# Kernel optimization log

Measured on AMD Instinct MI355X. Metric: run time of the kernel, lower is better.

## Reference

```python
import jax, jax.numpy as jnp
import numpy as np

N_NODES = 100000
N_EDGES = 1600000
IN_CH = 128
HID = 64
N_CLASSES = 16
N_GRAPHS = 64


def setup_inputs() -> dict:
    key = jax.random.key(0)
    ks = jax.random.split(key, 10)
    x = jax.random.normal(ks[0], (N_NODES, IN_CH), dtype=jnp.float32)
    edge_index = jax.random.randint(ks[1], (2, N_EDGES), 0, N_NODES, dtype=jnp.int64)
    edge_weight = jax.random.uniform(ks[2], (N_EDGES,), dtype=jnp.float32)
    batch = jnp.sort(jax.random.randint(ks[3], (N_NODES,), 0, N_GRAPHS, dtype=jnp.int64))
    s1 = 1.0 / np.sqrt(IN_CH)
    s2 = 1.0 / np.sqrt(HID)
    W1 = jax.random.uniform(ks[4], (IN_CH, HID), jnp.float32, -s1, s1)
    b1 = jnp.zeros((HID,), jnp.float32)
    W2 = jax.random.uniform(ks[5], (HID, HID), jnp.float32, -s2, s2)
    b2 = jnp.zeros((HID,), jnp.float32)
    Wl = jax.random.uniform(ks[6], (HID, N_CLASSES), jnp.float32, -s2, s2)
    bl = jax.random.uniform(ks[7], (N_CLASSES,), jnp.float32, -s2, s2)
    return {"x": x, "edge_index": edge_index, "edge_weight": edge_weight,
            "batch": batch, "W1": W1, "b1": b1, "W2": W2, "b2": b2,
            "Wl": Wl, "bl": bl}


def _gcn_conv(x, src, dst, ew, W, b, n_nodes):
    # PyG GCNConv: h = x @ W; symmetric normalization with self-loops;
    # out[dst] += norm * h[src]; out += bias.
    deg = jax.ops.segment_sum(ew, dst, num_segments=n_nodes)
    deg_inv_sqrt = jnp.where(deg > 0, jax.lax.rsqrt(jnp.maximum(deg, 1e-30)), 0.0)
    norm = deg_inv_sqrt[src] * ew * deg_inv_sqrt[dst]  # [E']
    h = x @ W                                          # [N, out]
    msg = h[src] * norm[:, None]                       # [E', out] gather
    out = jax.ops.segment_sum(msg, dst, num_segments=n_nodes)  # scatter-add
    return out + b


def reference(x, edge_index, edge_weight, batch, W1, b1, W2, b2, Wl, bl):
    n = x.shape[0]
    # add self loops once (weight 1.0), shared by both conv layers
    loop = jnp.arange(n, dtype=edge_index.dtype)
    src = jnp.concatenate([edge_index[0], loop])
    dst = jnp.concatenate([edge_index[1], loop])
    ew = jnp.concatenate([edge_weight, jnp.ones((n,), edge_weight.dtype)])

    h = jax.nn.relu(_gcn_conv(x, src, dst, ew, W1, b1, n))
    h = jax.nn.relu(_gcn_conv(h, src, dst, ew, W2, b2, n))

    # global_mean_pool over graphs
    sums = jax.ops.segment_sum(h, batch, num_segments=N_GRAPHS)  # [G, HID]
    cnt = jax.ops.segment_sum(jnp.ones((n,), h.dtype), batch, num_segments=N_GRAPHS)
    pooled = sums / jnp.maximum(cnt, 1.0)[:, None]

    return pooled @ Wl + bl
```

## Files before the change

### kernel.cpp

```cpp
#include <hip/hip_runtime.h>
#include <hip/hip_fp16.h>

#define N_NODES   100000
#define N_EDGES   1600000
#define IN_CH     128
#define HID       64
#define N_CLASSES 16
#define N_GRAPHS  64

#define BK_SH     9
#define BK_NODES  512
#define NB        ((N_NODES + BK_NODES - 1) / BK_NODES)
#define BK_CAP    10240
#define CH_EDGES  4096
#define EPT       16
#define NCH       ((N_EDGES + CH_EDGES - 1) / CH_EDGES)
#define AGG_NPW   2

typedef __attribute__((ext_vector_type(8))) short bf16x8;
typedef __attribute__((ext_vector_type(4))) float f32x4;
typedef __attribute__((ext_vector_type(4))) unsigned u32x4;
typedef __attribute__((ext_vector_type(2))) unsigned u32x2;

__device__ __forceinline__ unsigned short f2bf(float f) {
    unsigned u = __float_as_uint(f);
    u += 0x7fffu + ((u >> 16) & 1u);
    return (unsigned short)(u >> 16);
}
__device__ __forceinline__ f32x4 bf4v(uint2 v) {
    u32x4 u;
    u.x = v.x << 16; u.y = v.x & 0xffff0000u;
    u.z = v.y << 16; u.w = v.y & 0xffff0000u;
    return __builtin_bit_cast(f32x4, u);
}
__device__ __forceinline__ float dec_ew(unsigned v) {
    return __half2float(__ushort_as_half((unsigned short)(v >> 17)));
}

#if __has_builtin(__builtin_amdgcn_make_buffer_rsrc) && \
    __has_builtin(__builtin_amdgcn_raw_buffer_load_b32) && \
    __has_builtin(__builtin_amdgcn_raw_buffer_load_b64)
struct BufView {
    __amdgpu_buffer_rsrc_t rsrc;
    __device__ __forceinline__ void init(const void* p) {
        rsrc = __builtin_amdgcn_make_buffer_rsrc((void*)p, (short)0,
                                                 (int)0xFFFFFFFF, 0x00020000);
    }
    __device__ __forceinline__ unsigned ld32(unsigned off) const {
        return __builtin_amdgcn_raw_buffer_load_b32(rsrc, (int)off, 0, 0);
    }
    __device__ __forceinline__ uint2 ld64(unsigned off) const {
        u32x2 r = __builtin_amdgcn_raw_buffer_load_b64(rsrc, (int)off, 0, 0);
        return make_uint2(r.x, r.y);
    }
};
#else
struct BufView {
    const char* base;
    __device__ __forceinline__ void init(const void* p) { base = (const char*)p; }
    __device__ __forceinline__ unsigned ld32(unsigned off) const {
        return *(const unsigned*)(base + off);
    }
    __device__ __forceinline__ uint2 ld64(unsigned off) const {
        return *(const uint2*)(base + off);
    }
};
#endif

__global__ void k_init(int* __restrict__ bcursor, float* __restrict__ pooled) {
    int i = blockIdx.x * 256 + threadIdx.x;
    if (i < NB) bcursor[i] = i * BK_CAP;
    if (i < N_GRAPHS * HID) pooled[i] = 0.0f;
}

__global__ void k_binscatter(const int* __restrict__ src, const int* __restrict__ dst,
                             const float* __restrict__ ew, int* __restrict__ bcursor,
                             int2* __restrict__ bedges) {
    __shared__ int  hist[NB];
    __shared__ int  offs[NB];
    __shared__ int  gbase[NB];
    __shared__ int  sc[256];
    __shared__ int2 stage[CH_EDGES];
    __shared__ int  dest[CH_EDGES];
    const int t = threadIdx.x;
    const int base = blockIdx.x * CH_EDGES;
    const int nloc = min(CH_EDGES, N_EDGES - base);

    for (int i = t; i < NB; i += 256) hist[i] = 0;
    __syncthreads();

    int myb[EPT], myr[EPT], myp[EPT]; float myw[EPT];
#pragma unroll
    for (int j = 0; j < EPT; ++j) {
        int i = base + j * 256 + t;
        if (i < N_EDGES) {
            int s = src[i], d = dst[i];
            int b = d >> BK_SH;
            myb[j] = b;
            myr[j] = atomicAdd(&hist[b], 1);
            myp[j] = s | ((d & (BK_NODES - 1)) << 17);
            myw[j] = ew[i];
        } else {
            myb[j] = -1;
        }
    }
    __syncthreads();

    int v = (t < NB) ? hist[t] : 0;
    sc[t] = v;
    __syncthreads();
    for (int off = 1; off < 256; off <<= 1) {
        int a = (t >= off) ? sc[t - off] : 0;
        __syncthreads();
        sc[t] += a;
        __syncthreads();
    }
    if (t < NB) {
        offs[t] = sc[t] - v;
        gbase[t] = (v > 0) ? atomicAdd(&bcursor[t], v) : 0;
    }
    __syncthreads();

#pragma unroll
    for (int j = 0; j < EPT; ++j) {
        if (myb[j] >= 0) {
            int p = offs[myb[j]] + myr[j];
            stage[p] = make_int2(myp[j], __float_as_int(myw[j]));
            dest[p] = gbase[myb[j]] + myr[j];
        }
    }
    __syncthreads();

    for (int i = t; i < nloc; i += 256)
        bedges[dest[i]] = stage[i];
}

__global__ __launch_bounds__(256) void k_build(const int* __restrict__ bcursor,
                                               const int2* __restrict__ bedges,
                                               int2* __restrict__ rowse,
                                               float* __restrict__ dis,
                                               unsigned* __restrict__ csr) {
    __shared__ int2  eds[BK_CAP];
    __shared__ int   cnt[BK_NODES];
    __shared__ float dsum[BK_NODES];
    __shared__ int   cur[BK_NODES];
    __shared__ int   sc[256];
    const int b = blockIdx.x;
    const int t = threadIdx.x;
    const int beg = b * BK_CAP, end = bcursor[b];
    const int n = end - beg;

    for (int i = t; i < BK_NODES; i += 256) { cnt[i] = 0; dsum[i] = 0.0f; }
    __syncthreads();

    for (int i = t; i < n; i += 256) {
        int2 e = bedges[beg + i];
        eds[i] = e;
        int dl = ((unsigned)e.x) >> 17;
        atomicAdd(&cnt[dl], 1);
        atomicAdd(&dsum[dl], __int_as_float(e.y));
    }
    __syncthreads();

    int a0 = cnt[2 * t], a1 = cnt[2 * t + 1];
    int pair = a0 + a1;
    sc[t] = pair;
    __syncthreads();
    for (int off = 1; off < 256; off <<= 1) {
        int a = (t >= off) ? sc[t - off] : 0;
        __syncthreads();
        sc[t] += a;
        __syncthreads();
    }
    int excl = sc[t] - pair;
    cur[2 * t] = excl;
    cur[2 * t + 1] = excl + a0;
    {
        int n0 = b * BK_NODES + 2 * t;
        if (n0 < N_NODES) {
            rowse[n0] = make_int2(beg + excl, beg + excl + a0);
            dis[n0] = rsqrtf(1.0f + dsum[2 * t]);
        }
        int n1 = n0 + 1;
        if (n1 < N_NODES) {
            rowse[n1] = make_int2(beg + excl + a0, beg + excl + a0 + a1);
            dis[n1] = rsqrtf(1.0f + dsum[2 * t + 1]);
        }
    }
    __syncthreads();

    for (int i = t; i < n; i += 256) {
        int2 e = eds[i];
        int dl = ((unsigned)e.x) >> 17;
        int s = e.x & 0x1FFFF;
        unsigned short w16 = __half_as_ushort(__float2half(__int_as_float(e.y)));
        int pos = beg + atomicAdd(&cur[dl], 1);
        csr[pos] = (unsigned)s | ((unsigned)w16 << 17);
    }
}

template <int K, bool INB>
__global__ __launch_bounds__(256) void k_gemm(const float* __restrict__ x,
                                              const unsigned short* __restrict__ xb,
                                              const float* __restrict__ W,
                                              const float* __restrict__ dis,
                                              unsigned short* __restrict__ hb) {
    constexpr int AS = K + 8;
    __shared__ unsigned short wt[64 * AS];
    const int t    = threadIdx.x;
    const int lane = t & 63;
    const int wave = t >> 6;
    const int m    = lane & 15;
    const int quad = lane >> 4;
    const int rowbase = blockIdx.x * 64;

    bf16x8 afrag[K / 32];

    if constexpr (!INB) {
        __shared__ unsigned short a_s[64 * AS];
        constexpr int CPR = K / 8;
        for (int c = t; c < 64 * CPR; c += 256) {
            int row = c / CPR, cc = c % CPR;
            int gr = rowbase + row;
            float4 v0, v1;
            if (gr < N_NODES) {
                v0 = *(const float4*)&x[(long)gr * K + cc * 8];
                v1 = *(const float4*)&x[(long)gr * K + cc * 8 + 4];
            } else {
                v0 = make_float4(0.f, 0.f, 0.f, 0.f); v1 = v0;
            }
            uint4 p;
            p.x = f2bf(v0.x) | ((unsigned)f2bf(v0.y) << 16);
            p.y = f2bf(v0.z) | ((unsigned)f2bf(v0.w) << 16);
            p.z = f2bf(v1.x) | ((unsigned)f2bf(v1.y) << 16);
            p.w = f2bf(v1.z) | ((unsigned)f2bf(v1.w) << 16);
            *(uint4*)&a_s[row * AS + cc * 8] = p;
        }
        for (int idx = t; idx < K * 64; idx += 256) {
            int k = idx >> 6, n = idx & 63;
            wt[n * AS + k] = f2bf(W[idx]);
        }
        __syncthreads();
#pragma unroll
        for (int ks = 0; ks < K / 32; ++ks)
            afrag[ks] = *(const bf16x8*)&a_s[(wave * 16 + m) * AS + ks * 32 + quad * 8];
    } else {
        const int gr = rowbase + wave * 16 + m;
#pragma unroll
        for (int ks = 0; ks < K / 32; ++ks) {
            if (gr < N_NODES)
                afrag[ks] = *(const bf16x8*)&xb[(long)gr * K + ks * 32 + quad * 8];
            else
                afrag[ks] = (bf16x8){0, 0, 0, 0, 0, 0, 0, 0};
        }
        for (int idx = t; idx < K * 64; idx += 256) {
            int k = idx >> 6, n = idx & 63;
            wt[n * AS + k] = f2bf(W[idx]);
        }
        __syncthreads();
    }

    bf16x8 bfrag[4][K / 32];
#pragma unroll
    for (int nt = 0; nt < 4; ++nt)
#pragma unroll
        for (int ks = 0; ks < K / 32; ++ks)
            bfrag[nt][ks] = *(const bf16x8*)&wt[(nt * 16 + m) * AS + ks * 32 + quad * 8];

    f32x4 acc[4];
#pragma unroll
    for (int nt = 0; nt < 4; ++nt) acc[nt] = (f32x4){0.f, 0.f, 0.f, 0.f};

#pragma unroll
    for (int ks = 0; ks < K / 32; ++ks) {
#pragma unroll
        for (int nt = 0; nt < 4; ++nt)
            acc[nt] = __builtin_amdgcn_mfma_f32_16x16x32_bf16(afrag[ks], bfrag[nt][ks],
                                                              acc[nt], 0, 0, 0);
    }

#pragma unroll
    for (int i = 0; i < 4; ++i) {
        int gr = rowbase + wave * 16 + quad * 4 + i;
        if (gr < N_NODES) {
            float dsc = dis[gr];
#pragma unroll
            for (int nt = 0; nt < 4; ++nt)
                hb[(long)gr * HID + nt * 16 + m] = f2bf(dsc * acc[nt][i]);
        }
    }
}


#define FULLBLK(pX, eX, f_, x0, x1, x2, x3, accX)                             \
    do {                                                                      \
        const unsigned e0_ = x0, e1_ = x1, e2_ = x2, e3_ = x3;                \
        pX += 16;                                                             \
        f_ = (pX + 16 <= eX);                                                 \
        if (f_) {                                                             \
            const unsigned v_ = (unsigned)((pX + g) << 2);                    \
            x0 = vc.ld32(v_);      x1 = vc.ld32(v_ + 16);                     \
            x2 = vc.ld32(v_ + 32); x3 = vc.ld32(v_ + 48);                     \
        }                                                                     \
        f32x4 v0_ = bf4v(vh.ld64(((e0_ & 0x1FFFF) << 7) | coff));             \
        f32x4 v1_ = bf4v(vh.ld64(((e1_ & 0x1FFFF) << 7) | coff));             \
        f32x4 v2_ = bf4v(vh.ld64(((e2_ & 0x1FFFF) << 7) | coff));             \
        f32x4 v3_ = bf4v(vh.ld64(((e3_ & 0x1FFFF) << 7) | coff));             \
        accX += v0_ * dec_ew(e0_);                                            \
        accX += v1_ * dec_ew(e1_);                                            \
        accX += v2_ * dec_ew(e2_);                                            \
        accX += v3_ * dec_ew(e3_);                                            \
    } while (0)

template <bool OB>
__global__ void k_aggregate(const int2* __restrict__ rowse,
                            const unsigned* __restrict__ csr,
                            const uint2* __restrict__ hb, const float* __restrict__ dis,
                            const float* __restrict__ b, const int* __restrict__ batch,
                            float* __restrict__ pooled, uint2* __restrict__ outb) {
    __shared__ float psh[4 * AGG_NPW][HID];
    const int tid  = threadIdx.x;
    const int lane = tid & 63;
    const int g    = lane >> 4;
    const int c4   = lane & 15;
    const int wave = tid >> 6;
    const int node0 = (blockIdx.x * 4 + wave) * AGG_NPW;
    const int node1 = node0 + 1;
    const float4 bb = ((const float4*)b)[c4];
    const f32x4 bbv = {bb.x, bb.y, bb.z, bb.w};

    BufView vc; vc.init(csr);
    BufView vh; vh.init(hb);
    const unsigned coff = (unsigned)(c4 << 3);

    const int4 rr = *(const int4*)&rowse[node0];
    const uint2 hs0 = hb[node0 * 16 + c4];
    const uint2 hs1 = hb[node1 * 16 + c4];

    f32x4 acc0 = (g == 0) ? bf4v(hs0) : (f32x4){0.f, 0.f, 0.f, 0.f};
    f32x4 acc1 = (g == 0) ? bf4v(hs1) : (f32x4){0.f, 0.f, 0.f, 0.f};

    int p0 = rr.x; const int e0 = rr.y;
    int p1 = rr.z; const int e1 = rr.w;

    unsigned a0 = 0, a1 = 0, a2 = 0, a3 = 0;
    unsigned b0 = 0, b1 = 0, b2 = 0, b3 = 0;
    bool fA = (p0 + 16 <= e0);
    bool fB = (p1 + 16 <= e1);
    if (fA) {
        const unsigned v = (unsigned)((p0 + g) << 2);
        a0 = vc.ld32(v);      a1 = vc.ld32(v + 16);
        a2 = vc.ld32(v + 32); a3 = vc.ld32(v + 48);
    }
    if (fB) {
        const unsigned v = (unsigned)((p1 + g) << 2);
        b0 = vc.ld32(v);      b1 = vc.ld32(v + 16);
        b2 = vc.ld32(v + 32); b3 = vc.ld32(v + 48);
    }

    while (fA && fB) {
        FULLBLK(p0, e0, fA, a0, a1, a2, a3, acc0);
        FULLBLK(p1, e1, fB, b0, b1, b2, b3, acc1);
    }
    while (fA) FULLBLK(p0, e0, fA, a0, a1, a2, a3, acc0);
    while (fB) FULLBLK(p1, e1, fB, b0, b1, b2, b3, acc1);

    const bool tA = (p0 < e0);
    const bool tB = (p1 < e1);
    unsigned ta0 = 0, ta1 = 0, ta2 = 0, ta3 = 0;
    unsigned tb0 = 0, tb1 = 0, tb2 = 0, tb3 = 0;
    if (tA) {
        const int last = e0 - 1;
        ta0 = vc.ld32((unsigned)(min(p0 + g,      last) << 2));
        ta1 = vc.ld32((unsigned)(min(p0 + 4 + g,  last) << 2));
        ta2 = vc.ld32((unsigned)(min(p0 + 8 + g,  last) << 2));
        ta3 = vc.ld32((unsigned)(min(p0 + 12 + g, last) << 2));
    }
    if (tB) {
        const int last = e1 - 1;
        tb0 = vc.ld32((unsigned)(min(p1 + g,      last) << 2));
        tb1 = vc.ld32((unsigned)(min(p1 + 4 + g,  last) << 2));
        tb2 = vc.ld32((unsigned)(min(p1 + 8 + g,  last) << 2));
        tb3 = vc.ld32((unsigned)(min(p1 + 12 + g, last) << 2));
    }
    if (tA) {
        f32x4 v0 = bf4v(vh.ld64(((ta0 & 0x1FFFF) << 7) | coff));
        f32x4 v1 = bf4v(vh.ld64(((ta1 & 0x1FFFF) << 7) | coff));
        f32x4 v2 = bf4v(vh.ld64(((ta2 & 0x1FFFF) << 7) | coff));
        f32x4 v3 = bf4v(vh.ld64(((ta3 & 0x1FFFF) << 7) | coff));
        acc0 += v0 * ((p0 + g      < e0) ? dec_ew(ta0) : 0.f);
        acc0 += v1 * ((p0 + 4 + g  < e0) ? dec_ew(ta1) : 0.f);
        acc0 += v2 * ((p0 + 8 + g  < e0) ? dec_ew(ta2) : 0.f);
        acc0 += v3 * ((p0 + 12 + g < e0) ? dec_ew(ta3) : 0.f);
    }
    if (tB) {
        f32x4 v0 = bf4v(vh.ld64(((tb0 & 0x1FFFF) << 7) | coff));
        f32x4 v1 = bf4v(vh.ld64(((tb1 & 0x1FFFF) << 7) | coff));
        f32x4 v2 = bf4v(vh.ld64(((tb2 & 0x1FFFF) << 7) | coff));
        f32x4 v3 = bf4v(vh.ld64(((tb3 & 0x1FFFF) << 7) | coff));
        acc1 += v0 * ((p1 + g      < e1) ? dec_ew(tb0) : 0.f);
        acc1 += v1 * ((p1 + 4 + g  < e1) ? dec_ew(tb1) : 0.f);
        acc1 += v2 * ((p1 + 8 + g  < e1) ? dec_ew(tb2) : 0.f);
        acc1 += v3 * ((p1 + 12 + g < e1) ? dec_ew(tb3) : 0.f);
    }

#pragma unroll
    for (int i = 0; i < 4; ++i) {
        float t0 = acc0[i];
        t0 += __shfl_xor(t0, 16); t0 += __shfl_xor(t0, 32);
        acc0[i] = t0;
        float t1 = acc1[i];
        t1 += __shfl_xor(t1, 16); t1 += __shfl_xor(t1, 32);
        acc1[i] = t1;
    }

    if (g == 0) {
        const float dd0 = dis[node0];
        const float dd1 = dis[node1];
        f32x4 o0 = acc0 * dd0 + bbv;
        f32x4 o1 = acc1 * dd1 + bbv;
        o0.x = fmaxf(o0.x, 0.f); o0.y = fmaxf(o0.y, 0.f);
        o0.z = fmaxf(o0.z, 0.f); o0.w = fmaxf(o0.w, 0.f);
        o1.x = fmaxf(o1.x, 0.f); o1.y = fmaxf(o1.y, 0.f);
        o1.z = fmaxf(o1.z, 0.f); o1.w = fmaxf(o1.w, 0.f);
        if constexpr (OB) {
            uint2 pk0, pk1;
            pk0.x = (unsigned)f2bf(o0.x) | ((unsigned)f2bf(o0.y) << 16);
            pk0.y = (unsigned)f2bf(o0.z) | ((unsigned)f2bf(o0.w) << 16);
            pk1.x = (unsigned)f2bf(o1.x) | ((unsigned)f2bf(o1.y) << 16);
            pk1.y = (unsigned)f2bf(o1.z) | ((unsigned)f2bf(o1.w) << 16);
            outb[node0 * 16 + c4] = pk0;
            outb[node1 * 16 + c4] = pk1;
        } else {
            *(f32x4*)&psh[wave * AGG_NPW][c4 * 4] = o0;
            *(f32x4*)&psh[wave * AGG_NPW + 1][c4 * 4] = o1;
        }
    }

    if constexpr (!OB) {
        __syncthreads();
        if (tid < HID) {
            const int nb0 = blockIdx.x * 4 * AGG_NPW;
            int curg = batch[nb0];
            float a = 0.f;
#pragma unroll
            for (int j = 0; j < 4 * AGG_NPW; ++j) {
                int bg = batch[nb0 + j];
                if (bg != curg) {
                    atomicAdd(&pooled[curg * HID + tid], a);
                    a = 0.f; curg = bg;
                }
                a += psh[j][tid];
            }
            atomicAdd(&pooled[curg * HID + tid], a);
        }
    }
}

__global__ __launch_bounds__(1024) void k_out(const float* __restrict__ pooled,
                      const int* __restrict__ batch,
                      const float* __restrict__ Wl, const float* __restrict__ bl,
                      float* __restrict__ out) {
    __shared__ int bnd[N_GRAPHS + 1];
    int tid = threadIdx.x;
    if (tid <= N_GRAPHS) {
        int target = tid;
        int lo = 0, hi = N_NODES;
        while (lo < hi) {
            int mid = (lo + hi) >> 1;
            if (batch[mid] < target) lo = mid + 1; else hi = mid;
        }
        bnd[tid] = lo;
    }
    __syncthreads();
    int g = tid >> 4, k = tid & 15;
    float cntg = (float)(bnd[g + 1] - bnd[g]);
    float inv = 1.0f / fmaxf(cntg, 1.0f);
    float acc = 0.f;
#pragma unroll
    for (int h = 0; h < HID; ++h) acc += pooled[g * HID + h] * Wl[h * N_CLASSES + k];
    out[g * N_CLASSES + k] = acc * inv + bl[k];
}

extern "C" void kernel_launch(void* const* d_in, const int* in_sizes, int n_in,
                              void* d_out, int out_size, void* d_ws, size_t ws_size,
                              hipStream_t stream) {
    const float* x     = (const float*)d_in[0];
    const int*   ei    = (const int*)d_in[1];
    const float* ew    = (const float*)d_in[2];
    const int*   batch = (const int*)d_in[3];
    const float* W1    = (const float*)d_in[4];
    const float* b1    = (const float*)d_in[5];
    const float* W2    = (const float*)d_in[6];
    const float* b2    = (const float*)d_in[7];
    const float* Wl    = (const float*)d_in[8];
    const float* bl    = (const float*)d_in[9];

    const int* srcv = ei;
    const int* dstv = ei + N_EDGES;

    char* wsb = (char*)d_ws;
    float*          dis    = (float*)wsb;              wsb += 100352 * 4;
    int2*           rowse  = (int2*)wsb;               wsb += 100352 * 8;
    int*            bcursor= (int*)wsb;                wsb += 256 * 4;
    unsigned*       csr    = (unsigned*)wsb;           wsb += (size_t)NB * BK_CAP * 4;
    unsigned short* hb     = (unsigned short*)wsb;     wsb += N_NODES * HID * 2;
    char*           scratch= wsb;                      wsb += N_NODES * HID * 4;
    float*          pooled = (float*)wsb;              wsb += N_GRAPHS * HID * 4;
    float*          out    = (float*)d_out;
    int2*           bedges = (int2*)scratch;
    unsigned short* hbA    = (unsigned short*)scratch;

    k_init<<<16, 256, 0, stream>>>(bcursor, pooled);
    k_binscatter<<<NCH, 256, 0, stream>>>(srcv, dstv, ew, bcursor, bedges);
    k_build<<<NB, 256, 0, stream>>>(bcursor, bedges, rowse, dis, csr);

    const int agg_blocks = N_NODES / (4 * AGG_NPW);

    k_gemm<IN_CH, false><<<(N_NODES + 63) / 64, 256, 0, stream>>>(x, nullptr, W1, dis, hb);
    k_aggregate<true><<<agg_blocks, 256, 0, stream>>>(rowse, csr, (const uint2*)hb,
                                                      dis, b1, batch, nullptr, (uint2*)hbA);
    k_gemm<HID, true><<<(N_NODES + 63) / 64, 256, 0, stream>>>(nullptr, hbA, W2, dis, hb);
    k_aggregate<false><<<agg_blocks, 256, 0, stream>>>(rowse, csr, (const uint2*)hb,
                                                       dis, b2, batch, pooled, nullptr);

    k_out<<<1, 1024, 0, stream>>>(pooled, batch, Wl, bl, out);
}
```

Measured before the change: 255.8 us.

## Merge two nodes' edge ranges into one stream with up-front batched gathers

The aggregate kernel now treats the contiguous CSR span of both nodes of a wave as a single edge stream. Each 16-edge block is routed to acc0 or acc1, or split at the boundary using masked weights. The first two blocks and the tail are loaded and gathered up front, so more memory requests are in flight before any accumulation. The dis and batch values are prefetched early, and batch is read as two int4 vectors for the pooling step. The aim is to cut the dependent-load latency and loop overhead of the old dual-loop scheme, at the cost of more registers and extra per-block routing branches.

```diff
diff --git a/kernel.cpp b/kernel.cpp
--- a/kernel.cpp
+++ b/kernel.cpp
@@ -292,24 +292,36 @@
 }
 
 
-#define FULLBLK(pX, eX, f_, x0, x1, x2, x3, accX)                             \
+#define GATH4(x0_, x1_, x2_, x3_, q0_, q1_, q2_, q3_)                         \
     do {                                                                      \
-        const unsigned e0_ = x0, e1_ = x1, e2_ = x2, e3_ = x3;                \
-        pX += 16;                                                             \
-        f_ = (pX + 16 <= eX);                                                 \
-        if (f_) {                                                             \
-            const unsigned v_ = (unsigned)((pX + g) << 2);                    \
-            x0 = vc.ld32(v_);      x1 = vc.ld32(v_ + 16);                     \
-            x2 = vc.ld32(v_ + 32); x3 = vc.ld32(v_ + 48);                     \
+        q0_ = vh.ld64(((x0_ & 0x1FFFF) << 7) | coff);                         \
+        q1_ = vh.ld64(((x1_ & 0x1FFFF) << 7) | coff);                         \
+        q2_ = vh.ld64(((x2_ & 0x1FFFF) << 7) | coff);                         \
+        q3_ = vh.ld64(((x3_ & 0x1FFFF) << 7) | coff);                         \
+    } while (0)
+
+#define ROUTE4(pb_, x0_, x1_, x2_, x3_, q0_, q1_, q2_, q3_)                   \
+    do {                                                                      \
+        f32x4 v0_ = bf4v(q0_), v1_ = bf4v(q1_);                               \
+        f32x4 v2_ = bf4v(q2_), v3_ = bf4v(q3_);                               \
+        float w0_ = dec_ew(x0_), w1_ = dec_ew(x1_);                           \
+        float w2_ = dec_ew(x2_), w3_ = dec_ew(x3_);                           \
+        if (pb_ + 16 <= e0) {                                                 \
+            acc0 += v0_ * w0_; acc0 += v1_ * w1_;                             \
+            acc0 += v2_ * w2_; acc0 += v3_ * w3_;                             \
+        } else if (pb_ >= e0) {                                               \
+            acc1 += v0_ * w0_; acc1 += v1_ * w1_;                             \
+            acc1 += v2_ * w2_; acc1 += v3_ * w3_;                             \
+        } else {                                                              \
+            float a0_ = (pb_ + g      < e0) ? w0_ : 0.f;                      \
+            float a1_ = (pb_ + 4 + g  < e0) ? w1_ : 0.f;                      \
+            float a2_ = (pb_ + 8 + g  < e0) ? w2_ : 0.f;                      \
+            float a3_ = (pb_ + 12 + g < e0) ? w3_ : 0.f;                      \
+            acc0 += v0_ * a0_; acc1 += v0_ * (w0_ - a0_);                     \
+            acc0 += v1_ * a1_; acc1 += v1_ * (w1_ - a1_);                     \
+            acc0 += v2_ * a2_; acc1 += v2_ * (w2_ - a2_);                     \
+            acc0 += v3_ * a3_; acc1 += v3_ * (w3_ - a3_);                     \
         }                                                                     \
-        f32x4 v0_ = bf4v(vh.ld64(((e0_ & 0x1FFFF) << 7) | coff));             \
-        f32x4 v1_ = bf4v(vh.ld64(((e1_ & 0x1FFFF) << 7) | coff));             \
-        f32x4 v2_ = bf4v(vh.ld64(((e2_ & 0x1FFFF) << 7) | coff));             \
-        f32x4 v3_ = bf4v(vh.ld64(((e3_ & 0x1FFFF) << 7) | coff));             \
-        accX += v0_ * dec_ew(e0_);                                            \
-        accX += v1_ * dec_ew(e1_);                                            \
-        accX += v2_ * dec_ew(e2_);                                            \
-        accX += v3_ * dec_ew(e3_);                                            \
     } while (0)
 
 template <bool OB>
@@ -336,87 +348,99 @@
     const int4 rr = *(const int4*)&rowse[node0];
     const uint2 hs0 = hb[node0 * 16 + c4];
     const uint2 hs1 = hb[node1 * 16 + c4];
+    const float dd0 = dis[node0];
+    const float dd1 = dis[node1];
+    int4 bq0, bq1;
+    if constexpr (!OB) {
+        if (tid < HID) {
+            bq0 = ((const int4*)(batch + blockIdx.x * 4 * AGG_NPW))[0];
+            bq1 = ((const int4*)(batch + blockIdx.x * 4 * AGG_NPW))[1];
+        }
+    }
+
+    const int s  = __builtin_amdgcn_readfirstlane(rr.x);
+    const int e0 = __builtin_amdgcn_readfirstlane(rr.y);
+    const int e1 = __builtin_amdgcn_readfirstlane(rr.w);
 
     f32x4 acc0 = (g == 0) ? bf4v(hs0) : (f32x4){0.f, 0.f, 0.f, 0.f};
     f32x4 acc1 = (g == 0) ? bf4v(hs1) : (f32x4){0.f, 0.f, 0.f, 0.f};
 
-    int p0 = rr.x; const int e0 = rr.y;
-    int p1 = rr.z; const int e1 = rr.w;
-
-    unsigned a0 = 0, a1 = 0, a2 = 0, a3 = 0;
-    unsigned b0 = 0, b1 = 0, b2 = 0, b3 = 0;
-    bool fA = (p0 + 16 <= e0);
-    bool fB = (p1 + 16 <= e1);
-    if (fA) {
-        const unsigned v = (unsigned)((p0 + g) << 2);
-        a0 = vc.ld32(v);      a1 = vc.ld32(v + 16);
-        a2 = vc.ld32(v + 32); a3 = vc.ld32(v + 48);
-    }
-    if (fB) {
-        const unsigned v = (unsigned)((p1 + g) << 2);
-        b0 = vc.ld32(v);      b1 = vc.ld32(v + 16);
-        b2 = vc.ld32(v + 32); b3 = vc.ld32(v + 48);
-    }
-
-    while (fA && fB) {
-        FULLBLK(p0, e0, fA, a0, a1, a2, a3, acc0);
-        FULLBLK(p1, e1, fB, b0, b1, b2, b3, acc1);
-    }
-    while (fA) FULLBLK(p0, e0, fA, a0, a1, a2, a3, acc0);
-    while (fB) FULLBLK(p1, e1, fB, b0, b1, b2, b3, acc1);
-
-    const bool tA = (p0 < e0);
-    const bool tB = (p1 < e1);
-    unsigned ta0 = 0, ta1 = 0, ta2 = 0, ta3 = 0;
-    unsigned tb0 = 0, tb1 = 0, tb2 = 0, tb3 = 0;
-    if (tA) {
-        const int last = e0 - 1;
-        ta0 = vc.ld32((unsigned)(min(p0 + g,      last) << 2));
-        ta1 = vc.ld32((unsigned)(min(p0 + 4 + g,  last) << 2));
-        ta2 = vc.ld32((unsigned)(min(p0 + 8 + g,  last) << 2));
-        ta3 = vc.ld32((unsigned)(min(p0 + 12 + g, last) << 2));
-    }
-    if (tB) {
+    const int nf = (e1 - s) >> 4;
+    const int pt = s + (nf << 4);
+    const bool h0 = (nf >= 1);
+    const bool h1 = (nf >= 2);
+    const bool hm = (nf > 2);
+    const bool ht = (pt < e1);
+
+    unsigned c0 = 0, c1 = 0, c2 = 0, c3 = 0;
+    unsigned d0 = 0, d1 = 0, d2 = 0, d3 = 0;
+    unsigned t0 = 0, t1 = 0, t2 = 0, t3 = 0;
+    if (h0) {
+        const unsigned v = (unsigned)((s + g) << 2);
+        c0 = vc.ld32(v);      c1 = vc.ld32(v + 16);
+        c2 = vc.ld32(v + 32); c3 = vc.ld32(v + 48);
+    }
+    if (h1) {
+        const unsigned v = (unsigned)((s + 16 + g) << 2);
+        d0 = vc.ld32(v);      d1 = vc.ld32(v + 16);
+        d2 = vc.ld32(v + 32); d3 = vc.ld32(v + 48);
+    }
+    if (ht) {
         const int last = e1 - 1;
-        tb0 = vc.ld32((unsigned)(min(p1 + g,      last) << 2));
-        tb1 = vc.ld32((unsigned)(min(p1 + 4 + g,  last) << 2));
-        tb2 = vc.ld32((unsigned)(min(p1 + 8 + g,  last) << 2));
-        tb3 = vc.ld32((unsigned)(min(p1 + 12 + g, last) << 2));
-    }
-    if (tA) {
-        f32x4 v0 = bf4v(vh.ld64(((ta0 & 0x1FFFF) << 7) | coff));
-        f32x4 v1 = bf4v(vh.ld64(((ta1 & 0x1FFFF) << 7) | coff));
-        f32x4 v2 = bf4v(vh.ld64(((ta2 & 0x1FFFF) << 7) | coff));
-        f32x4 v3 = bf4v(vh.ld64(((ta3 & 0x1FFFF) << 7) | coff));
-        acc0 += v0 * ((p0 + g      < e0) ? dec_ew(ta0) : 0.f);
-        acc0 += v1 * ((p0 + 4 + g  < e0) ? dec_ew(ta1) : 0.f);
-        acc0 += v2 * ((p0 + 8 + g  < e0) ? dec_ew(ta2) : 0.f);
-        acc0 += v3 * ((p0 + 12 + g < e0) ? dec_ew(ta3) : 0.f);
-    }
-    if (tB) {
-        f32x4 v0 = bf4v(vh.ld64(((tb0 & 0x1FFFF) << 7) | coff));
-        f32x4 v1 = bf4v(vh.ld64(((tb1 & 0x1FFFF) << 7) | coff));
-        f32x4 v2 = bf4v(vh.ld64(((tb2 & 0x1FFFF) << 7) | coff));
-        f32x4 v3 = bf4v(vh.ld64(((tb3 & 0x1FFFF) << 7) | coff));
-        acc1 += v0 * ((p1 + g      < e1) ? dec_ew(tb0) : 0.f);
-        acc1 += v1 * ((p1 + 4 + g  < e1) ? dec_ew(tb1) : 0.f);
-        acc1 += v2 * ((p1 + 8 + g  < e1) ? dec_ew(tb2) : 0.f);
-        acc1 += v3 * ((p1 + 12 + g < e1) ? dec_ew(tb3) : 0.f);
+        t0 = vc.ld32((unsigned)(min(pt + g,      last) << 2));
+        t1 = vc.ld32((unsigned)(min(pt + 4 + g,  last) << 2));
+        t2 = vc.ld32((unsigned)(min(pt + 8 + g,  last) << 2));
+        t3 = vc.ld32((unsigned)(min(pt + 12 + g, last) << 2));
+    }
+
+    uint2 r00, r01, r02, r03, r10, r11, r12, r13, rt0, rt1, rt2, rt3;
+    if (h0) GATH4(c0, c1, c2, c3, r00, r01, r02, r03);
+    if (h1) GATH4(d0, d1, d2, d3, r10, r11, r12, r13);
+    if (ht) GATH4(t0, t1, t2, t3, rt0, rt1, rt2, rt3);
+
+    if (h0) ROUTE4(s,      c0, c1, c2, c3, r00, r01, r02, r03);
+    if (h1) ROUTE4(s + 16, d0, d1, d2, d3, r10, r11, r12, r13);
+
+    if (hm) {
+        for (int p = s + 32; p + 16 <= e1; p += 16) {
+            unsigned m0, m1, m2, m3;
+            uint2 q0, q1, q2, q3;
+            const unsigned v = (unsigned)((p + g) << 2);
+            m0 = vc.ld32(v);      m1 = vc.ld32(v + 16);
+            m2 = vc.ld32(v + 32); m3 = vc.ld32(v + 48);
+            GATH4(m0, m1, m2, m3, q0, q1, q2, q3);
+            ROUTE4(p, m0, m1, m2, m3, q0, q1, q2, q3);
+        }
+    }
+
+    if (ht) {
+        f32x4 v0 = bf4v(rt0), v1 = bf4v(rt1), v2 = bf4v(rt2), v3 = bf4v(rt3);
+        const int i0 = pt + g, i1 = pt + 4 + g, i2 = pt + 8 + g, i3 = pt + 12 + g;
+        float w0 = (i0 < e1) ? dec_ew(t0) : 0.f;
+        float w1 = (i1 < e1) ? dec_ew(t1) : 0.f;
+        float w2 = (i2 < e1) ? dec_ew(t2) : 0.f;
+        float w3 = (i3 < e1) ? dec_ew(t3) : 0.f;
+        float a0 = (i0 < e0) ? w0 : 0.f;
+        float a1 = (i1 < e0) ? w1 : 0.f;
+        float a2 = (i2 < e0) ? w2 : 0.f;
+        float a3 = (i3 < e0) ? w3 : 0.f;
+        acc0 += v0 * a0; acc1 += v0 * (w0 - a0);
+        acc0 += v1 * a1; acc1 += v1 * (w1 - a1);
+        acc0 += v2 * a2; acc1 += v2 * (w2 - a2);
+        acc0 += v3 * a3; acc1 += v3 * (w3 - a3);
     }
 
 #pragma unroll
     for (int i = 0; i < 4; ++i) {
-        float t0 = acc0[i];
-        t0 += __shfl_xor(t0, 16); t0 += __shfl_xor(t0, 32);
-        acc0[i] = t0;
-        float t1 = acc1[i];
-        t1 += __shfl_xor(t1, 16); t1 += __shfl_xor(t1, 32);
-        acc1[i] = t1;
+        float u0 = acc0[i];
+        u0 += __shfl_xor(u0, 16); u0 += __shfl_xor(u0, 32);
+        acc0[i] = u0;
+        float u1 = acc1[i];
+        u1 += __shfl_xor(u1, 16); u1 += __shfl_xor(u1, 32);
+        acc1[i] = u1;
     }
 
     if (g == 0) {
-        const float dd0 = dis[node0];
-        const float dd1 = dis[node1];
         f32x4 o0 = acc0 * dd0 + bbv;
         f32x4 o1 = acc1 * dd1 + bbv;
         o0.x = fmaxf(o0.x, 0.f); o0.y = fmaxf(o0.y, 0.f);
@@ -440,18 +464,17 @@
     if constexpr (!OB) {
         __syncthreads();
         if (tid < HID) {
-            const int nb0 = blockIdx.x * 4 * AGG_NPW;
-            int curg = batch[nb0];
-            float a = 0.f;
-#pragma unroll
-            for (int j = 0; j < 4 * AGG_NPW; ++j) {
-                int bg = batch[nb0 + j];
-                if (bg != curg) {
-                    atomicAdd(&pooled[curg * HID + tid], a);
-                    a = 0.f; curg = bg;
-                }
-                a += psh[j][tid];
-            }
+            float a = psh[0][tid];
+            int curg = bq0.x;
+#define PSTEP(bg_, j_)                                                        \
+            if (bg_ != curg) {                                                \
+                atomicAdd(&pooled[curg * HID + tid], a);                      \
+                a = 0.f; curg = bg_;                                          \
+            }                                                                 \
+            a += psh[j_][tid];
+            PSTEP(bq0.y, 1) PSTEP(bq0.z, 2) PSTEP(bq0.w, 3)
+            PSTEP(bq1.x, 4) PSTEP(bq1.y, 5) PSTEP(bq1.z, 6) PSTEP(bq1.w, 7)
+#undef PSTEP
             atomicAdd(&pooled[curg * HID + tid], a);
         }
     }
```

New measurement: 262.2 us. 2.5% more time.

## Fuse second-layer GEMM into first aggregation kernel epilogue

Applied to the files above, without the earlier changes.

The layer-1 aggregation kernel now loads W2 into shared memory, stages each wave's two output rows in LDS, and runs a small MFMA to produce the layer-2 projected features (scaled by deg^-1/2) directly. This removes the separate k_gemm<HID> launch and the round trip of the intermediate activations through global memory. The cost is that every aggregation block converts and stores the full W2 tile in LDS, adding an extra barrier and using an MFMA that fills only 2 of 16 rows. Higher LDS use may also lower occupancy of the gather-bound kernel.

```diff
diff --git a/kernel.cpp b/kernel.cpp
--- a/kernel.cpp
+++ b/kernel.cpp
@@ -199,14 +199,14 @@
     }
 }
 
-template <int K, bool INB>
+template <int K>
 __global__ __launch_bounds__(256) void k_gemm(const float* __restrict__ x,
-                                              const unsigned short* __restrict__ xb,
                                               const float* __restrict__ W,
                                               const float* __restrict__ dis,
                                               unsigned short* __restrict__ hb) {
     constexpr int AS = K + 8;
     __shared__ unsigned short wt[64 * AS];
+    __shared__ unsigned short a_s[64 * AS];
     const int t    = threadIdx.x;
     const int lane = t & 63;
     const int wave = t >> 6;
@@ -214,51 +214,34 @@
     const int quad = lane >> 4;
     const int rowbase = blockIdx.x * 64;
 
+    constexpr int CPR = K / 8;
+    for (int c = t; c < 64 * CPR; c += 256) {
+        int row = c / CPR, cc = c % CPR;
+        int gr = rowbase + row;
+        float4 v0, v1;
+        if (gr < N_NODES) {
+            v0 = *(const float4*)&x[(long)gr * K + cc * 8];
+            v1 = *(const float4*)&x[(long)gr * K + cc * 8 + 4];
+        } else {
+            v0 = make_float4(0.f, 0.f, 0.f, 0.f); v1 = v0;
+        }
+        uint4 p;
+        p.x = f2bf(v0.x) | ((unsigned)f2bf(v0.y) << 16);
+        p.y = f2bf(v0.z) | ((unsigned)f2bf(v0.w) << 16);
+        p.z = f2bf(v1.x) | ((unsigned)f2bf(v1.y) << 16);
+        p.w = f2bf(v1.z) | ((unsigned)f2bf(v1.w) << 16);
+        *(uint4*)&a_s[row * AS + cc * 8] = p;
+    }
+    for (int idx = t; idx < K * 64; idx += 256) {
+        int k = idx >> 6, n = idx & 63;
+        wt[n * AS + k] = f2bf(W[idx]);
+    }
+    __syncthreads();
+
     bf16x8 afrag[K / 32];
-
-    if constexpr (!INB) {
-        __shared__ unsigned short a_s[64 * AS];
-        constexpr int CPR = K / 8;
-        for (int c = t; c < 64 * CPR; c += 256) {
-            int row = c / CPR, cc = c % CPR;
-            int gr = rowbase + row;
-            float4 v0, v1;
-            if (gr < N_NODES) {
-                v0 = *(const float4*)&x[(long)gr * K + cc * 8];
-                v1 = *(const float4*)&x[(long)gr * K + cc * 8 + 4];
-            } else {
-                v0 = make_float4(0.f, 0.f, 0.f, 0.f); v1 = v0;
-            }
-            uint4 p;
-            p.x = f2bf(v0.x) | ((unsigned)f2bf(v0.y) << 16);
-            p.y = f2bf(v0.z) | ((unsigned)f2bf(v0.w) << 16);
-            p.z = f2bf(v1.x) | ((unsigned)f2bf(v1.y) << 16);
-            p.w = f2bf(v1.z) | ((unsigned)f2bf(v1.w) << 16);
-            *(uint4*)&a_s[row * AS + cc * 8] = p;
-        }
-        for (int idx = t; idx < K * 64; idx += 256) {
-            int k = idx >> 6, n = idx & 63;
-            wt[n * AS + k] = f2bf(W[idx]);
-        }
-        __syncthreads();
-#pragma unroll
-        for (int ks = 0; ks < K / 32; ++ks)
-            afrag[ks] = *(const bf16x8*)&a_s[(wave * 16 + m) * AS + ks * 32 + quad * 8];
-    } else {
-        const int gr = rowbase + wave * 16 + m;
-#pragma unroll
-        for (int ks = 0; ks < K / 32; ++ks) {
-            if (gr < N_NODES)
-                afrag[ks] = *(const bf16x8*)&xb[(long)gr * K + ks * 32 + quad * 8];
-            else
-                afrag[ks] = (bf16x8){0, 0, 0, 0, 0, 0, 0, 0};
-        }
-        for (int idx = t; idx < K * 64; idx += 256) {
-            int k = idx >> 6, n = idx & 63;
-            wt[n * AS + k] = f2bf(W[idx]);
-        }
-        __syncthreads();
-    }
+#pragma unroll
+    for (int ks = 0; ks < K / 32; ++ks)
+        afrag[ks] = *(const bf16x8*)&a_s[(wave * 16 + m) * AS + ks * 32 + quad * 8];
 
     bf16x8 bfrag[4][K / 32];
 #pragma unroll
@@ -317,8 +300,13 @@
                             const unsigned* __restrict__ csr,
                             const uint2* __restrict__ hb, const float* __restrict__ dis,
                             const float* __restrict__ b, const int* __restrict__ batch,
-                            float* __restrict__ pooled, uint2* __restrict__ outb) {
+                            float* __restrict__ pooled,
+                            unsigned short* __restrict__ hb2,
+                            const float* __restrict__ W2) {
     __shared__ float psh[4 * AGG_NPW][HID];
+    __shared__ unsigned short wt2[64 * (HID + 8)];
+    __shared__ unsigned short prow[8][HID];
+    constexpr int AS2 = HID + 8;
     const int tid  = threadIdx.x;
     const int lane = tid & 63;
     const int g    = lane >> 4;
@@ -328,6 +316,14 @@
     const int node1 = node0 + 1;
     const float4 bb = ((const float4*)b)[c4];
     const f32x4 bbv = {bb.x, bb.y, bb.z, bb.w};
+
+    if constexpr (OB) {
+        for (int idx = tid; idx < HID * 64; idx += 256) {
+            int k = idx >> 6, n = idx & 63;
+            wt2[n * AS2 + k] = f2bf(W2[idx]);
+        }
+        __syncthreads();
+    }
 
     BufView vc; vc.init(csr);
     BufView vh; vh.init(hb);
@@ -414,26 +410,56 @@
         acc1[i] = t1;
     }
 
+    const float dd0 = dis[node0];
+    const float dd1 = dis[node1];
+
     if (g == 0) {
-        const float dd0 = dis[node0];
-        const float dd1 = dis[node1];
         f32x4 o0 = acc0 * dd0 + bbv;
         f32x4 o1 = acc1 * dd1 + bbv;
         o0.x = fmaxf(o0.x, 0.f); o0.y = fmaxf(o0.y, 0.f);
         o0.z = fmaxf(o0.z, 0.f); o0.w = fmaxf(o0.w, 0.f);
         o1.x = fmaxf(o1.x, 0.f); o1.y = fmaxf(o1.y, 0.f);
         o1.z = fmaxf(o1.z, 0.f); o1.w = fmaxf(o1.w, 0.f);
+        uint2 pk0, pk1;
+        pk0.x = (unsigned)f2bf(o0.x) | ((unsigned)f2bf(o0.y) << 16);
+        pk0.y = (unsigned)f2bf(o0.z) | ((unsigned)f2bf(o0.w) << 16);
+        pk1.x = (unsigned)f2bf(o1.x) | ((unsigned)f2bf(o1.y) << 16);
+        pk1.y = (unsigned)f2bf(o1.z) | ((unsigned)f2bf(o1.w) << 16);
         if constexpr (OB) {
-            uint2 pk0, pk1;
-            pk0.x = (unsigned)f2bf(o0.x) | ((unsigned)f2bf(o0.y) << 16);
-            pk0.y = (unsigned)f2bf(o0.z) | ((unsigned)f2bf(o0.w) << 16);
-            pk1.x = (unsigned)f2bf(o1.x) | ((unsigned)f2bf(o1.y) << 16);
-            pk1.y = (unsigned)f2bf(o1.z) | ((unsigned)f2bf(o1.w) << 16);
-            outb[node0 * 16 + c4] = pk0;
-            outb[node1 * 16 + c4] = pk1;
+            ((uint2*)prow)[(wave * 2) * 16 + c4]     = pk0;
+            ((uint2*)prow)[(wave * 2 + 1) * 16 + c4] = pk1;
         } else {
             *(f32x4*)&psh[wave * AGG_NPW][c4 * 4] = o0;
             *(f32x4*)&psh[wave * AGG_NPW + 1][c4 * 4] = o1;
+        }
+    }
+
+    if constexpr (OB) {
+        __syncthreads();
+        const int mm = lane & 15;
+        const int qq = lane >> 4;
+        const int arow = wave * 2 + (mm < 2 ? mm : 0);
+        bf16x8 af0 = *(const bf16x8*)&prow[arow][qq * 8];
+        bf16x8 af1 = *(const bf16x8*)&prow[arow][32 + qq * 8];
+        f32x4 a2[4];
+#pragma unroll
+        for (int nt = 0; nt < 4; ++nt) a2[nt] = (f32x4){0.f, 0.f, 0.f, 0.f};
+#pragma unroll
+        for (int nt = 0; nt < 4; ++nt) {
+            bf16x8 bf0 = *(const bf16x8*)&wt2[(nt * 16 + mm) * AS2 + qq * 8];
+            a2[nt] = __builtin_amdgcn_mfma_f32_16x16x32_bf16(af0, bf0, a2[nt], 0, 0, 0);
+        }
+#pragma unroll
+        for (int nt = 0; nt < 4; ++nt) {
+            bf16x8 bf1 = *(const bf16x8*)&wt2[(nt * 16 + mm) * AS2 + 32 + qq * 8];
+            a2[nt] = __builtin_amdgcn_mfma_f32_16x16x32_bf16(af1, bf1, a2[nt], 0, 0, 0);
+        }
+        if (qq == 0) {
+#pragma unroll
+            for (int nt = 0; nt < 4; ++nt) {
+                hb2[(size_t)node0 * HID + nt * 16 + mm] = f2bf(dd0 * a2[nt][0]);
+                hb2[(size_t)node1 * HID + nt * 16 + mm] = f2bf(dd1 * a2[nt][1]);
+            }
         }
     }
 
@@ -509,7 +535,7 @@
     float*          pooled = (float*)wsb;              wsb += N_GRAPHS * HID * 4;
     float*          out    = (float*)d_out;
     int2*           bedges = (int2*)scratch;
-    unsigned short* hbA    = (unsigned short*)scratch;
+    unsigned short* hb2    = (unsigned short*)scratch;
 
     k_init<<<16, 256, 0, stream>>>(bcursor, pooled);
     k_binscatter<<<NCH, 256, 0, stream>>>(srcv, dstv, ew, bcursor, bedges);
@@ -517,12 +543,12 @@
 
     const int agg_blocks = N_NODES / (4 * AGG_NPW);
 
-    k_gemm<IN_CH, false><<<(N_NODES + 63) / 64, 256, 0, stream>>>(x, nullptr, W1, dis, hb);
+    k_gemm<IN_CH><<<(N_NODES + 63) / 64, 256, 0, stream>>>(x, W1, dis, hb);
     k_aggregate<true><<<agg_blocks, 256, 0, stream>>>(rowse, csr, (const uint2*)hb,
-                                                      dis, b1, batch, nullptr, (uint2*)hbA);
-    k_gemm<HID, true><<<(N_NODES + 63) / 64, 256, 0, stream>>>(nullptr, hbA, W2, dis, hb);
-    k_aggregate<false><<<agg_blocks, 256, 0, stream>>>(rowse, csr, (const uint2*)hb,
-                                                       dis, b2, batch, pooled, nullptr);
+                                                      dis, b1, batch, nullptr, hb2, W2);
+    k_aggregate<false><<<agg_blocks, 256, 0, stream>>>(rowse, csr, (const uint2*)hb2,
+                                                       dis, b2, batch, pooled,
+                                                       nullptr, nullptr);
 
     k_out<<<1, 1024, 0, stream>>>(pooled, batch, Wl, bl, out);
 }
```

Result: no change. 254.2 us (-0.6%).
